# Kernel tuning notes

Hardware: AMD Instinct MI355X
Metric: run time of the kernel (lower is better)

## Reference

```python
import jax, jax.numpy as jnp
import numpy as np

EMBED_DIM = 512
NUM_HEADS = 8
HEAD_DIM = EMBED_DIM // NUM_HEADS
SCALING = HEAD_DIM ** (-0.5)
LAMBDA = 1.0
T = 128
B = 8


def setup_inputs() -> dict:
    key = jax.random.key(0)
    ks = jax.random.split(key, 8)
    d = EMBED_DIM
    # xavier-uniform-ish scale for weights
    w_lim = float(np.sqrt(6.0 / (3 * d + d)))
    o_lim = float(np.sqrt(6.0 / (d + d)))
    return {
        "query": jax.random.normal(ks[0], (T, B, d), jnp.float32),
        "key": jax.random.normal(ks[1], (T, B, d), jnp.float32),
        "value": jax.random.normal(ks[2], (T, B, d), jnp.float32),
        "correlation_bias": jax.random.normal(ks[3], (B, T, T, T), jnp.float32) * 0.1,
        "in_proj_weight": jax.random.uniform(ks[4], (3 * d, d), jnp.float32, -w_lim, w_lim),
        "in_proj_bias": jnp.zeros((3 * d,), jnp.float32),
        "out_w": jax.random.uniform(ks[5], (d, d), jnp.float32, -o_lim, o_lim),
        "out_b": jnp.zeros((d,), jnp.float32),
    }


def reference(query, key, value, correlation_bias, in_proj_weight, in_proj_bias, out_w, out_b):
    tgt_len, bsz, d = query.shape
    h, hd = NUM_HEADS, HEAD_DIM
    # split packed in-projection
    q = query @ in_proj_weight[:d].T + in_proj_bias[:d]
    k = key @ in_proj_weight[d:2 * d].T + in_proj_bias[d:2 * d]
    v = value @ in_proj_weight[2 * d:].T + in_proj_bias[2 * d:]
    q = q * SCALING
    # [T, B, D] -> [B*H, T, hd]
    q = q.reshape(tgt_len, bsz * h, hd).transpose(1, 0, 2)
    k = k.reshape(tgt_len, bsz * h, hd).transpose(1, 0, 2)
    v = v.reshape(tgt_len, bsz * h, hd).transpose(1, 0, 2)
    # trilinear score cube: [B*H, Tq, Tk, Tv]
    scores = jnp.einsum('iat,ibt,ict->iabc', q, k, v)
    # expand correlation bias over heads: [B,Tq,Tk,Tv] -> [B*H,Tq,Tk,Tv]
    bias = jnp.broadcast_to(
        correlation_bias[:, None], (bsz, h, tgt_len, tgt_len, tgt_len)
    ).reshape(bsz * h, tgt_len, tgt_len, tgt_len)
    scores = scores + LAMBDA * bias
    # mean/max fusion over Tv, softmax over Tk
    fused = jnp.mean(scores, axis=-1) + jnp.max(scores, axis=-1)
    w = jax.nn.softmax(fused.astype(jnp.float32), axis=-1).astype(fused.dtype)
    # bmm with q (note: attends over q itself, Tk == Tq required)
    attn = jnp.einsum('iab,ibd->iad', w, q)
    attn = attn.transpose(1, 0, 2).reshape(tgt_len, bsz, d)
    return attn @ out_w.T + out_b
```

## Files before the change

kernel.cpp:

```cpp
#include <hip/hip_runtime.h>
#include <math.h>

#define SCALING 0.125f

typedef __attribute__((ext_vector_type(8))) short short8;
typedef __attribute__((ext_vector_type(4))) float f32x4;

static __device__ __forceinline__ unsigned short bf16r(float x) {
  unsigned int u = __float_as_uint(x);
  u += 0x7fffu + ((u >> 16) & 1u);
  return (unsigned short)(u >> 16);
}
static __device__ __forceinline__ float bf16f(unsigned short h) {
  return __uint_as_float(((unsigned int)h) << 16);
}
static __device__ __forceinline__ unsigned int pk_bf16(float lo, float hi) {
  unsigned int ua = __float_as_uint(lo);
  unsigned int ub = __float_as_uint(hi);
  ua += 0x7fffu + ((ua >> 16) & 1u);
  ub += 0x7fffu + ((ub >> 16) & 1u);
  return __builtin_amdgcn_perm(ub, ua, 0x07060302u);
}
static __device__ __forceinline__ void split4(float4 x, ushort4& h, ushort4& l) {
  h.x = bf16r(x.x); l.x = bf16r(x.x - bf16f(h.x));
  h.y = bf16r(x.y); l.y = bf16r(x.y - bf16f(h.y));
  h.z = bf16r(x.z); l.z = bf16r(x.z - bf16f(h.z));
  h.w = bf16r(x.w); l.w = bf16r(x.w - bf16f(h.w));
}
union U4S8 { uint4 u; short8 s; };

__global__ __launch_bounds__(256)
void projmm_kernel(const float* __restrict__ query,
                   const float* __restrict__ key,
                   const float* __restrict__ value,
                   const float* __restrict__ W,
                   const float* __restrict__ bias,
                   float* __restrict__ qh, float* __restrict__ kh,
                   unsigned short* __restrict__ vh) {
  __shared__ __align__(16) unsigned short Ah[64 * 72];
  __shared__ __align__(16) unsigned short Al[64 * 72];
  __shared__ __align__(16) unsigned short Bh[64 * 72];
  __shared__ __align__(16) unsigned short Bl[64 * 72];
  const int n0 = blockIdx.x * 64;
  const int g = n0 >> 9;
  const float* __restrict__ X = (g == 0) ? query : (g == 1) ? key : value;
  const int m0 = blockIdx.y * 64;
  const int tid = threadIdx.x;
  const int w = tid >> 6, lane = tid & 63;
  const int quad = lane >> 4, n15 = lane & 15;
  const int srow = tid >> 2;
  const int scol = (tid & 3) * 16;

  f32x4 acc[4];
#pragma unroll
  for (int nt = 0; nt < 4; ++nt) acc[nt] = (f32x4){0.f, 0.f, 0.f, 0.f};

  float4 av[4], bv[4];
#pragma unroll
  for (int jj = 0; jj < 4; ++jj) {
    av[jj] = *(const float4*)&X[(m0 + srow) * 512 + scol + 4 * jj];
    bv[jj] = *(const float4*)&W[(n0 + srow) * 512 + scol + 4 * jj];
  }

  for (int k0 = 0; k0 < 512; k0 += 64) {
    __syncthreads();
#pragma unroll
    for (int jj = 0; jj < 4; ++jj) {
      ushort4 hh, ll;
      split4(av[jj], hh, ll);
      *(ushort4*)&Ah[srow * 72 + scol + 4 * jj] = hh;
      *(ushort4*)&Al[srow * 72 + scol + 4 * jj] = ll;
      split4(bv[jj], hh, ll);
      *(ushort4*)&Bh[srow * 72 + scol + 4 * jj] = hh;
      *(ushort4*)&Bl[srow * 72 + scol + 4 * jj] = ll;
    }
    __syncthreads();
    if (k0 + 64 < 512) {
#pragma unroll
      for (int jj = 0; jj < 4; ++jj) {
        av[jj] = *(const float4*)&X[(m0 + srow) * 512 + k0 + 64 + scol + 4 * jj];
        bv[jj] = *(const float4*)&W[(n0 + srow) * 512 + k0 + 64 + scol + 4 * jj];
      }
    }
#pragma unroll
    for (int kk = 0; kk < 2; ++kk) {
      short8 ah = *(const short8*)&Ah[(w * 16 + n15) * 72 + kk * 32 + quad * 8];
      short8 al = *(const short8*)&Al[(w * 16 + n15) * 72 + kk * 32 + quad * 8];
#pragma unroll
      for (int nt = 0; nt < 4; ++nt) {
        short8 bh = *(const short8*)&Bh[(nt * 16 + n15) * 72 + kk * 32 + quad * 8];
        short8 bl = *(const short8*)&Bl[(nt * 16 + n15) * 72 + kk * 32 + quad * 8];
        acc[nt] = __builtin_amdgcn_mfma_f32_16x16x32_bf16(ah, bh, acc[nt], 0, 0, 0);
        acc[nt] = __builtin_amdgcn_mfma_f32_16x16x32_bf16(ah, bl, acc[nt], 0, 0, 0);
        acc[nt] = __builtin_amdgcn_mfma_f32_16x16x32_bf16(al, bh, acc[nt], 0, 0, 0);
      }
    }
  }

#pragma unroll
  for (int nt = 0; nt < 4; ++nt) {
    const int j = n0 + nt * 16 + n15;
    const int jj = j & 511;
    const int head = jj >> 6;
    const int hd = jj & 63;
    const float bj = bias[j];
#pragma unroll
    for (int r = 0; r < 4; ++r) {
      const int row = m0 + w * 16 + quad * 4 + r;
      const int t = row >> 3;
      const int batch = row & 7;
      const int i = batch * 8 + head;
      const int idx = ((i << 7) + t) * 64 + hd;
      const float val = acc[nt][r] + bj;
      if (g == 0)      qh[idx] = val * SCALING;
      else if (g == 1) kh[idx] = val;
      else             vh[idx] = bf16r(val);
    }
  }
}

__global__ __launch_bounds__(256, 2)
void score_kernel(const float* __restrict__ qh,
                  const float* __restrict__ kh,
                  const unsigned short* __restrict__ vh,
                  const float* __restrict__ cbias,
                  float* __restrict__ attn) {
  __shared__ __align__(16) unsigned short Ks[2][128 * 72];
  __shared__ __align__(16) unsigned short Vs[2][128 * 72];
  __shared__ float rowS[8 * 128];

  const int ab = blockIdx.x;
  const int batch = ab >> 7;
  const int a = ab & 127;
  const int tid = threadIdx.x;
  const int w = tid >> 6;
  const int lane = tid & 63;
  const int quad = lane >> 4;
  const int n15 = lane & 15;
  const int col8 = (tid & 7) * 8;

  const float* __restrict__ bp = cbias + (size_t)ab * 16384;
  f32x4 biasReg[8][2];
#pragma unroll
  for (int ic = 0; ic < 8; ++ic)
#pragma unroll
    for (int jb = 0; jb < 2; ++jb) {
      const int b = w * 32 + jb * 16 + n15;
      biasReg[ic][jb] = *(const f32x4*)&bp[b * 128 + ic * 16 + quad * 4];
    }

  {
    const int i = batch * 8;
    const float* __restrict__ kb = kh + (size_t)i * 8192;
    const uint4* __restrict__ vb4 = (const uint4*)(vh + (size_t)i * 8192);
    const float* __restrict__ qa = qh + ((size_t)i * 128 + a) * 64;
    f32x4 q0 = *(const f32x4*)&qa[col8];
    f32x4 q1 = *(const f32x4*)&qa[col8 + 4];
#pragma unroll
    for (int j = 0; j < 4; ++j) {
      const int gg = j * 256 + tid;
      const int row = gg >> 3;
      *(uint4*)&Vs[0][row * 72 + col8] = vb4[gg];
      f32x4 k0 = *(const f32x4*)&kb[8 * gg];
      f32x4 k1 = *(const f32x4*)&kb[8 * gg + 4];
      k0 *= q0;
      k1 *= q1;
      uint4 pk;
      pk.x = pk_bf16(k0[0], k0[1]); pk.y = pk_bf16(k0[2], k0[3]);
      pk.z = pk_bf16(k1[0], k1[1]); pk.w = pk_bf16(k1[2], k1[3]);
      *(uint4*)&Ks[0][row * 72 + col8] = pk;
    }
  }
  __syncthreads();

  for (int h = 0; h < 8; ++h) {
    const int buf = h & 1;
    const int i = batch * 8 + h;

    uint4 vreg[4];
    f32x4 kreg[4][2];
    f32x4 qn0, qn1;
    if (h < 7) {
      const int in = i + 1;
      const float* __restrict__ kb = kh + (size_t)in * 8192;
      const uint4* __restrict__ vb4 = (const uint4*)(vh + (size_t)in * 8192);
      const float* __restrict__ qa = qh + ((size_t)in * 128 + a) * 64;
      qn0 = *(const f32x4*)&qa[col8];
      qn1 = *(const f32x4*)&qa[col8 + 4];
#pragma unroll
      for (int j = 0; j < 4; ++j) {
        const int gg = j * 256 + tid;
        vreg[j] = vb4[gg];
        kreg[j][0] = *(const f32x4*)&kb[8 * gg];
        kreg[j][1] = *(const f32x4*)&kb[8 * gg + 4];
      }
    }

    short8 bf[2][2];
#pragma unroll
    for (int jb = 0; jb < 2; ++jb)
#pragma unroll
      for (int kk = 0; kk < 2; ++kk)
        bf[jb][kk] = *(const short8*)&Ks[buf][(w * 32 + jb * 16 + n15) * 72 +
                                             kk * 32 + quad * 8];

    f32x4 acc[8][2];
#pragma unroll
    for (int ic = 0; ic < 8; ++ic)
#pragma unroll
      for (int jb = 0; jb < 2; ++jb) acc[ic][jb] = (f32x4){0.f, 0.f, 0.f, 0.f};
#pragma unroll
    for (int ic = 0; ic < 8; ++ic) {
      short8 a0 = *(const short8*)&Vs[buf][(ic * 16 + n15) * 72 + quad * 8];
      short8 a1 = *(const short8*)&Vs[buf][(ic * 16 + n15) * 72 + 32 + quad * 8];
      acc[ic][0] = __builtin_amdgcn_mfma_f32_16x16x32_bf16(a0, bf[0][0], acc[ic][0], 0, 0, 0);
      acc[ic][0] = __builtin_amdgcn_mfma_f32_16x16x32_bf16(a1, bf[0][1], acc[ic][0], 0, 0, 0);
      acc[ic][1] = __builtin_amdgcn_mfma_f32_16x16x32_bf16(a0, bf[1][0], acc[ic][1], 0, 0, 0);
      acc[ic][1] = __builtin_amdgcn_mfma_f32_16x16x32_bf16(a1, bf[1][1], acc[ic][1], 0, 0, 0);
    }

    if (h < 7) {
      const int nb = buf ^ 1;
#pragma unroll
      for (int j = 0; j < 4; ++j) {
        const int gg = j * 256 + tid;
        const int row = gg >> 3;
        *(uint4*)&Vs[nb][row * 72 + col8] = vreg[j];
        kreg[j][0] *= qn0;
        kreg[j][1] *= qn1;
        uint4 pk;
        pk.x = pk_bf16(kreg[j][0][0], kreg[j][0][1]);
        pk.y = pk_bf16(kreg[j][0][2], kreg[j][0][3]);
        pk.z = pk_bf16(kreg[j][1][0], kreg[j][1][1]);
        pk.w = pk_bf16(kreg[j][1][2], kreg[j][1][3]);
        *(uint4*)&Ks[nb][row * 72 + col8] = pk;
      }
    }

    float fsum[2] = {0.f, 0.f};
    float fmx[2] = {-INFINITY, -INFINITY};
#pragma unroll
    for (int ic = 0; ic < 8; ++ic)
#pragma unroll
      for (int jb = 0; jb < 2; ++jb) {
        const float v0 = acc[ic][jb][0] + biasReg[ic][jb][0];
        const float v1 = acc[ic][jb][1] + biasReg[ic][jb][1];
        const float v2 = acc[ic][jb][2] + biasReg[ic][jb][2];
        const float v3 = acc[ic][jb][3] + biasReg[ic][jb][3];
        fsum[jb] += (v0 + v1) + (v2 + v3);
        fmx[jb] = fmaxf(fmx[jb], fmaxf(fmaxf(v0, v1), fmaxf(v2, v3)));
      }
#pragma unroll
    for (int off = 16; off <= 32; off <<= 1) {
#pragma unroll
      for (int jb = 0; jb < 2; ++jb) {
        fsum[jb] += __shfl_xor(fsum[jb], off, 64);
        fmx[jb] = fmaxf(fmx[jb], __shfl_xor(fmx[jb], off, 64));
      }
    }
    if (quad == 0) {
      rowS[h * 128 + w * 32 + n15] = fsum[0] * (1.0f / 128.0f) + fmx[0];
      rowS[h * 128 + w * 32 + 16 + n15] = fsum[1] * (1.0f / 128.0f) + fmx[1];
    }

    __syncthreads();
  }

#pragma unroll
  for (int hh = 0; hh < 2; ++hh) {
    const int h = w * 2 + hh;
    const int i = batch * 8 + h;
    float f0 = rowS[h * 128 + lane], f1 = rowS[h * 128 + 64 + lane];
    float m = fmaxf(f0, f1);
#pragma unroll
    for (int off = 32; off >= 1; off >>= 1) m = fmaxf(m, __shfl_xor(m, off, 64));
    const float e0 = expf(f0 - m), e1 = expf(f1 - m);
    float s = e0 + e1;
#pragma unroll
    for (int off = 32; off >= 1; off >>= 1) s += __shfl_xor(s, off, 64);
    const float inv = 1.0f / s;
    rowS[h * 128 + lane] = e0 * inv;
    rowS[h * 128 + 64 + lane] = e1 * inv;
    const float* __restrict__ qp = qh + (size_t)i * 8192 + lane;
    float acc2 = 0.0f;
#pragma unroll 8
    for (int b = 0; b < 128; ++b)
      acc2 = fmaf(rowS[h * 128 + b], qp[b * 64], acc2);
    attn[((size_t)a * 8 + batch) * 512 + h * 64 + lane] = acc2;
  }
}

__global__ __launch_bounds__(256)
void outmm_kernel(const float* __restrict__ Xa,
                  const float* __restrict__ W,
                  const float* __restrict__ bias,
                  float* __restrict__ out) {
  __shared__ __align__(16) unsigned short Ah[64 * 72];
  __shared__ __align__(16) unsigned short Al[64 * 72];
  __shared__ __align__(16) unsigned short Bh[32 * 72];
  __shared__ __align__(16) unsigned short Bl[32 * 72];
  const int n0 = blockIdx.x * 32;
  const int m0 = blockIdx.y * 64;
  const int tid = threadIdx.x;
  const int w = tid >> 6, lane = tid & 63;
  const int quad = lane >> 4, n15 = lane & 15;
  const int srow = tid >> 2;
  const int scol = (tid & 3) * 16;
  const bool doB = tid >= 128;
  const int brow = (tid & 127) >> 2;
  const int bcol = (tid & 3) * 16;

  f32x4 acc[2];
#pragma unroll
  for (int nt = 0; nt < 2; ++nt) acc[nt] = (f32x4){0.f, 0.f, 0.f, 0.f};

  float4 av[4], bv[4];
#pragma unroll
  for (int jj = 0; jj < 4; ++jj)
    av[jj] = *(const float4*)&Xa[(m0 + srow) * 512 + scol + 4 * jj];
  if (doB) {
#pragma unroll
    for (int jj = 0; jj < 4; ++jj)
      bv[jj] = *(const float4*)&W[(n0 + brow) * 512 + bcol + 4 * jj];
  }

  for (int k0 = 0; k0 < 512; k0 += 64) {
    __syncthreads();
#pragma unroll
    for (int jj = 0; jj < 4; ++jj) {
      ushort4 hh, ll;
      split4(av[jj], hh, ll);
      *(ushort4*)&Ah[srow * 72 + scol + 4 * jj] = hh;
      *(ushort4*)&Al[srow * 72 + scol + 4 * jj] = ll;
    }
    if (doB) {
#pragma unroll
      for (int jj = 0; jj < 4; ++jj) {
        ushort4 hh, ll;
        split4(bv[jj], hh, ll);
        *(ushort4*)&Bh[brow * 72 + bcol + 4 * jj] = hh;
        *(ushort4*)&Bl[brow * 72 + bcol + 4 * jj] = ll;
      }
    }
    __syncthreads();
    if (k0 + 64 < 512) {
#pragma unroll
      for (int jj = 0; jj < 4; ++jj)
        av[jj] = *(const float4*)&Xa[(m0 + srow) * 512 + k0 + 64 + scol + 4 * jj];
      if (doB) {
#pragma unroll
        for (int jj = 0; jj < 4; ++jj)
          bv[jj] = *(const float4*)&W[(n0 + brow) * 512 + k0 + 64 + bcol + 4 * jj];
      }
    }
#pragma unroll
    for (int kk = 0; kk < 2; ++kk) {
      short8 ah = *(const short8*)&Ah[(w * 16 + n15) * 72 + kk * 32 + quad * 8];
      short8 al = *(const short8*)&Al[(w * 16 + n15) * 72 + kk * 32 + quad * 8];
#pragma unroll
      for (int nt = 0; nt < 2; ++nt) {
        short8 bh = *(const short8*)&Bh[(nt * 16 + n15) * 72 + kk * 32 + quad * 8];
        short8 bl = *(const short8*)&Bl[(nt * 16 + n15) * 72 + kk * 32 + quad * 8];
        acc[nt] = __builtin_amdgcn_mfma_f32_16x16x32_bf16(ah, bh, acc[nt], 0, 0, 0);
        acc[nt] = __builtin_amdgcn_mfma_f32_16x16x32_bf16(ah, bl, acc[nt], 0, 0, 0);
        acc[nt] = __builtin_amdgcn_mfma_f32_16x16x32_bf16(al, bh, acc[nt], 0, 0, 0);
      }
    }
  }

#pragma unroll
  for (int nt = 0; nt < 2; ++nt) {
    const int j = n0 + nt * 16 + n15;
    const float bj = bias[j];
#pragma unroll
    for (int r = 0; r < 4; ++r) {
      const int row = m0 + w * 16 + quad * 4 + r;
      out[(size_t)row * 512 + j] = acc[nt][r] + bj;
    }
  }
}

extern "C" void kernel_launch(void* const* d_in, const int* in_sizes, int n_in,
                              void* d_out, int out_size, void* d_ws,
                              size_t ws_size, hipStream_t stream) {
  const float* query = (const float*)d_in[0];
  const float* key   = (const float*)d_in[1];
  const float* value = (const float*)d_in[2];
  const float* cbias = (const float*)d_in[3];
  const float* W     = (const float*)d_in[4];
  const float* pb    = (const float*)d_in[5];
  const float* out_w = (const float*)d_in[6];
  const float* out_b = (const float*)d_in[7];
  float* out = (float*)d_out;

  float* ws = (float*)d_ws;
  float* qh = ws;
  float* kh = ws + 524288;
  unsigned short* vh = (unsigned short*)(ws + 1048576);
  float* attn = ws + 1048576 + 262144;

  projmm_kernel<<<dim3(24, 16), 256, 0, stream>>>(query, key, value, W, pb,
                                                  qh, kh, vh);
  score_kernel<<<1024, 256, 0, stream>>>(qh, kh, vh, cbias, attn);
  outmm_kernel<<<dim3(16, 16), 256, 0, stream>>>(attn, out_w, out_b, out);
}
```

Baseline: 187.2 us.

## Double score-kernel waves, keep K·q fragments in registers, seed MFMA with bias

```diff
diff --git a/kernel.cpp b/kernel.cpp
--- a/kernel.cpp
+++ b/kernel.cpp
@@ -119,13 +119,12 @@
   }
 }
 
-__global__ __launch_bounds__(256, 2)
+__global__ __launch_bounds__(512, 4)
 void score_kernel(const float* __restrict__ qh,
                   const float* __restrict__ kh,
                   const unsigned short* __restrict__ vh,
                   const float* __restrict__ cbias,
                   float* __restrict__ attn) {
-  __shared__ __align__(16) unsigned short Ks[2][128 * 72];
   __shared__ __align__(16) unsigned short Vs[2][128 * 72];
   __shared__ float rowS[8 * 128];
 
@@ -138,137 +137,106 @@
   const int quad = lane >> 4;
   const int n15 = lane & 15;
   const int col8 = (tid & 7) * 8;
+  const int brow = w * 16 + n15;
 
   const float* __restrict__ bp = cbias + (size_t)ab * 16384;
-  f32x4 biasReg[8][2];
+  f32x4 biasReg[8];
 #pragma unroll
   for (int ic = 0; ic < 8; ++ic)
-#pragma unroll
-    for (int jb = 0; jb < 2; ++jb) {
-      const int b = w * 32 + jb * 16 + n15;
-      biasReg[ic][jb] = *(const f32x4*)&bp[b * 128 + ic * 16 + quad * 4];
-    }
-
+    biasReg[ic] = *(const f32x4*)&bp[brow * 128 + ic * 16 + quad * 4];
+
+  short8 bf0, bf1;
   {
     const int i = batch * 8;
     const float* __restrict__ kb = kh + (size_t)i * 8192;
+    const float* __restrict__ qa = qh + ((size_t)i * 128 + a) * 64;
+    f32x4 k0a = *(const f32x4*)&kb[brow * 64 + quad * 8];
+    f32x4 k0b = *(const f32x4*)&kb[brow * 64 + quad * 8 + 4];
+    f32x4 k1a = *(const f32x4*)&kb[brow * 64 + 32 + quad * 8];
+    f32x4 k1b = *(const f32x4*)&kb[brow * 64 + 32 + quad * 8 + 4];
+    f32x4 q0a = *(const f32x4*)&qa[quad * 8];
+    f32x4 q0b = *(const f32x4*)&qa[quad * 8 + 4];
+    f32x4 q1a = *(const f32x4*)&qa[32 + quad * 8];
+    f32x4 q1b = *(const f32x4*)&qa[32 + quad * 8 + 4];
+    k0a *= q0a; k0b *= q0b; k1a *= q1a; k1b *= q1b;
+    U4S8 u0, u1;
+    u0.u.x = pk_bf16(k0a[0], k0a[1]); u0.u.y = pk_bf16(k0a[2], k0a[3]);
+    u0.u.z = pk_bf16(k0b[0], k0b[1]); u0.u.w = pk_bf16(k0b[2], k0b[3]);
+    u1.u.x = pk_bf16(k1a[0], k1a[1]); u1.u.y = pk_bf16(k1a[2], k1a[3]);
+    u1.u.z = pk_bf16(k1b[0], k1b[1]); u1.u.w = pk_bf16(k1b[2], k1b[3]);
+    bf0 = u0.s; bf1 = u1.s;
     const uint4* __restrict__ vb4 = (const uint4*)(vh + (size_t)i * 8192);
-    const float* __restrict__ qa = qh + ((size_t)i * 128 + a) * 64;
-    f32x4 q0 = *(const f32x4*)&qa[col8];
-    f32x4 q1 = *(const f32x4*)&qa[col8 + 4];
-#pragma unroll
-    for (int j = 0; j < 4; ++j) {
-      const int gg = j * 256 + tid;
-      const int row = gg >> 3;
-      *(uint4*)&Vs[0][row * 72 + col8] = vb4[gg];
-      f32x4 k0 = *(const f32x4*)&kb[8 * gg];
-      f32x4 k1 = *(const f32x4*)&kb[8 * gg + 4];
-      k0 *= q0;
-      k1 *= q1;
-      uint4 pk;
-      pk.x = pk_bf16(k0[0], k0[1]); pk.y = pk_bf16(k0[2], k0[3]);
-      pk.z = pk_bf16(k1[0], k1[1]); pk.w = pk_bf16(k1[2], k1[3]);
-      *(uint4*)&Ks[0][row * 72 + col8] = pk;
-    }
+    *(uint4*)&Vs[0][(tid >> 3) * 72 + col8] = vb4[tid];
+    *(uint4*)&Vs[0][(64 + (tid >> 3)) * 72 + col8] = vb4[512 + tid];
   }
   __syncthreads();
 
   for (int h = 0; h < 8; ++h) {
     const int buf = h & 1;
-    const int i = batch * 8 + h;
-
-    uint4 vreg[4];
-    f32x4 kreg[4][2];
-    f32x4 qn0, qn1;
+
+    uint4 vreg0, vreg1;
+    f32x4 kr0a, kr0b, kr1a, kr1b, qr0a, qr0b, qr1a, qr1b;
     if (h < 7) {
-      const int in = i + 1;
+      const int in = batch * 8 + h + 1;
       const float* __restrict__ kb = kh + (size_t)in * 8192;
+      const float* __restrict__ qa = qh + ((size_t)in * 128 + a) * 64;
       const uint4* __restrict__ vb4 = (const uint4*)(vh + (size_t)in * 8192);
-      const float* __restrict__ qa = qh + ((size_t)in * 128 + a) * 64;
-      qn0 = *(const f32x4*)&qa[col8];
-      qn1 = *(const f32x4*)&qa[col8 + 4];
-#pragma unroll
-      for (int j = 0; j < 4; ++j) {
-        const int gg = j * 256 + tid;
-        vreg[j] = vb4[gg];
-        kreg[j][0] = *(const f32x4*)&kb[8 * gg];
-        kreg[j][1] = *(const f32x4*)&kb[8 * gg + 4];
-      }
-    }
-
-    short8 bf[2][2];
-#pragma unroll
-    for (int jb = 0; jb < 2; ++jb)
-#pragma unroll
-      for (int kk = 0; kk < 2; ++kk)
-        bf[jb][kk] = *(const short8*)&Ks[buf][(w * 32 + jb * 16 + n15) * 72 +
-                                             kk * 32 + quad * 8];
-
-    f32x4 acc[8][2];
-#pragma unroll
-    for (int ic = 0; ic < 8; ++ic)
-#pragma unroll
-      for (int jb = 0; jb < 2; ++jb) acc[ic][jb] = (f32x4){0.f, 0.f, 0.f, 0.f};
+      vreg0 = vb4[tid];
+      vreg1 = vb4[512 + tid];
+      kr0a = *(const f32x4*)&kb[brow * 64 + quad * 8];
+      kr0b = *(const f32x4*)&kb[brow * 64 + quad * 8 + 4];
+      kr1a = *(const f32x4*)&kb[brow * 64 + 32 + quad * 8];
+      kr1b = *(const f32x4*)&kb[brow * 64 + 32 + quad * 8 + 4];
+      qr0a = *(const f32x4*)&qa[quad * 8];
+      qr0b = *(const f32x4*)&qa[quad * 8 + 4];
+      qr1a = *(const f32x4*)&qa[32 + quad * 8];
+      qr1b = *(const f32x4*)&qa[32 + quad * 8 + 4];
+    }
+
+    f32x4 acc[8];
 #pragma unroll
     for (int ic = 0; ic < 8; ++ic) {
       short8 a0 = *(const short8*)&Vs[buf][(ic * 16 + n15) * 72 + quad * 8];
       short8 a1 = *(const short8*)&Vs[buf][(ic * 16 + n15) * 72 + 32 + quad * 8];
-      acc[ic][0] = __builtin_amdgcn_mfma_f32_16x16x32_bf16(a0, bf[0][0], acc[ic][0], 0, 0, 0);
-      acc[ic][0] = __builtin_amdgcn_mfma_f32_16x16x32_bf16(a1, bf[0][1], acc[ic][0], 0, 0, 0);
-      acc[ic][1] = __builtin_amdgcn_mfma_f32_16x16x32_bf16(a0, bf[1][0], acc[ic][1], 0, 0, 0);
-      acc[ic][1] = __builtin_amdgcn_mfma_f32_16x16x32_bf16(a1, bf[1][1], acc[ic][1], 0, 0, 0);
+      f32x4 t = __builtin_amdgcn_mfma_f32_16x16x32_bf16(a0, bf0, biasReg[ic], 0, 0, 0);
+      acc[ic] = __builtin_amdgcn_mfma_f32_16x16x32_bf16(a1, bf1, t, 0, 0, 0);
     }
 
     if (h < 7) {
       const int nb = buf ^ 1;
-#pragma unroll
-      for (int j = 0; j < 4; ++j) {
-        const int gg = j * 256 + tid;
-        const int row = gg >> 3;
-        *(uint4*)&Vs[nb][row * 72 + col8] = vreg[j];
-        kreg[j][0] *= qn0;
-        kreg[j][1] *= qn1;
-        uint4 pk;
-        pk.x = pk_bf16(kreg[j][0][0], kreg[j][0][1]);
-        pk.y = pk_bf16(kreg[j][0][2], kreg[j][0][3]);
-        pk.z = pk_bf16(kreg[j][1][0], kreg[j][1][1]);
-        pk.w = pk_bf16(kreg[j][1][2], kreg[j][1][3]);
-        *(uint4*)&Ks[nb][row * 72 + col8] = pk;
-      }
-    }
-
-    float fsum[2] = {0.f, 0.f};
-    float fmx[2] = {-INFINITY, -INFINITY};
-#pragma unroll
-    for (int ic = 0; ic < 8; ++ic)
-#pragma unroll
-      for (int jb = 0; jb < 2; ++jb) {
-        const float v0 = acc[ic][jb][0] + biasReg[ic][jb][0];
-        const float v1 = acc[ic][jb][1] + biasReg[ic][jb][1];
-        const float v2 = acc[ic][jb][2] + biasReg[ic][jb][2];
-        const float v3 = acc[ic][jb][3] + biasReg[ic][jb][3];
-        fsum[jb] += (v0 + v1) + (v2 + v3);
-        fmx[jb] = fmaxf(fmx[jb], fmaxf(fmaxf(v0, v1), fmaxf(v2, v3)));
-      }
-#pragma unroll
-    for (int off = 16; off <= 32; off <<= 1) {
-#pragma unroll
-      for (int jb = 0; jb < 2; ++jb) {
-        fsum[jb] += __shfl_xor(fsum[jb], off, 64);
-        fmx[jb] = fmaxf(fmx[jb], __shfl_xor(fmx[jb], off, 64));
-      }
-    }
-    if (quad == 0) {
-      rowS[h * 128 + w * 32 + n15] = fsum[0] * (1.0f / 128.0f) + fmx[0];
-      rowS[h * 128 + w * 32 + 16 + n15] = fsum[1] * (1.0f / 128.0f) + fmx[1];
-    }
-
-    __syncthreads();
-  }
-
-#pragma unroll
-  for (int hh = 0; hh < 2; ++hh) {
-    const int h = w * 2 + hh;
+      *(uint4*)&Vs[nb][(tid >> 3) * 72 + col8] = vreg0;
+      *(uint4*)&Vs[nb][(64 + (tid >> 3)) * 72 + col8] = vreg1;
+      kr0a *= qr0a; kr0b *= qr0b; kr1a *= qr1a; kr1b *= qr1b;
+      U4S8 u0, u1;
+      u0.u.x = pk_bf16(kr0a[0], kr0a[1]); u0.u.y = pk_bf16(kr0a[2], kr0a[3]);
+      u0.u.z = pk_bf16(kr0b[0], kr0b[1]); u0.u.w = pk_bf16(kr0b[2], kr0b[3]);
+      u1.u.x = pk_bf16(kr1a[0], kr1a[1]); u1.u.y = pk_bf16(kr1a[2], kr1a[3]);
+      u1.u.z = pk_bf16(kr1b[0], kr1b[1]); u1.u.w = pk_bf16(kr1b[2], kr1b[3]);
+      bf0 = u0.s; bf1 = u1.s;
+    }
+
+    float fsum = 0.f;
+    float fmx = -INFINITY;
+#pragma unroll
+    for (int ic = 0; ic < 8; ++ic) {
+      const float v0 = acc[ic][0];
+      const float v1 = acc[ic][1];
+      const float v2 = acc[ic][2];
+      const float v3 = acc[ic][3];
+      fsum += (v0 + v1) + (v2 + v3);
+      fmx = fmaxf(fmx, fmaxf(fmaxf(v0, v1), fmaxf(v2, v3)));
+    }
+    fsum += __shfl_xor(fsum, 16, 64);
+    fmx = fmaxf(fmx, __shfl_xor(fmx, 16, 64));
+    fsum += __shfl_xor(fsum, 32, 64);
+    fmx = fmaxf(fmx, __shfl_xor(fmx, 32, 64));
+    if (quad == 0) rowS[h * 128 + w * 16 + n15] = fsum * (1.0f / 128.0f) + fmx;
+
+    __syncthreads();
+  }
+
+  {
+    const int h = w;
     const int i = batch * 8 + h;
     float f0 = rowS[h * 128 + lane], f1 = rowS[h * 128 + 64 + lane];
     float m = fmaxf(f0, f1);
@@ -401,6 +369,6 @@
 
   projmm_kernel<<<dim3(24, 16), 256, 0, stream>>>(query, key, value, W, pb,
                                                   qh, kh, vh);
-  score_kernel<<<1024, 256, 0, stream>>>(qh, kh, vh, cbias, attn);
+  score_kernel<<<1024, 512, 0, stream>>>(qh, kh, vh, cbias, attn);
   outmm_kernel<<<dim3(16, 16), 256, 0, stream>>>(attn, out_w, out_b, out);
 }
```

After: 194.2 us. 1.04x slower.

## Pre-split fp32 inputs and weights into bf16 hi/lo once before GEMMs

Applied to the files above, without the earlier changes.

```diff
diff --git a/kernel.cpp b/kernel.cpp
--- a/kernel.cpp
+++ b/kernel.cpp
@@ -30,10 +30,44 @@
 union U4S8 { uint4 u; short8 s; };
 
 __global__ __launch_bounds__(256)
-void projmm_kernel(const float* __restrict__ query,
-                   const float* __restrict__ key,
-                   const float* __restrict__ value,
-                   const float* __restrict__ W,
+void prep_kernel(const float* __restrict__ query,
+                 const float* __restrict__ key,
+                 const float* __restrict__ value,
+                 const float* __restrict__ W,
+                 const float* __restrict__ out_w,
+                 unsigned short* __restrict__ Xh,
+                 unsigned short* __restrict__ Xl,
+                 unsigned short* __restrict__ Wh,
+                 unsigned short* __restrict__ Wl,
+                 unsigned short* __restrict__ Owh,
+                 unsigned short* __restrict__ Owl) {
+  const int t = blockIdx.x * 256 + threadIdx.x;
+  const int e = t * 4;
+  const float* __restrict__ src;
+  unsigned short *dh, *dl;
+  if (e < 1572864) {
+    const int g = e >> 19, j = e & 524287;
+    src = (g == 0 ? query : g == 1 ? key : value) + j;
+    dh = Xh + e; dl = Xl + e;
+  } else if (e < 2359296) {
+    const int j = e - 1572864;
+    src = W + j; dh = Wh + j; dl = Wl + j;
+  } else {
+    const int j = e - 2359296;
+    src = out_w + j; dh = Owh + j; dl = Owl + j;
+  }
+  const float4 v = *(const float4*)src;
+  ushort4 hh, ll;
+  split4(v, hh, ll);
+  *(ushort4*)dh = hh;
+  *(ushort4*)dl = ll;
+}
+
+__global__ __launch_bounds__(256)
+void projmm_kernel(const unsigned short* __restrict__ Xh,
+                   const unsigned short* __restrict__ Xl,
+                   const unsigned short* __restrict__ Wh,
+                   const unsigned short* __restrict__ Wl,
                    const float* __restrict__ bias,
                    float* __restrict__ qh, float* __restrict__ kh,
                    unsigned short* __restrict__ vh) {
@@ -43,7 +77,8 @@
   __shared__ __align__(16) unsigned short Bl[64 * 72];
   const int n0 = blockIdx.x * 64;
   const int g = n0 >> 9;
-  const float* __restrict__ X = (g == 0) ? query : (g == 1) ? key : value;
+  const unsigned short* __restrict__ Xgh = Xh + g * 524288;
+  const unsigned short* __restrict__ Xgl = Xl + g * 524288;
   const int m0 = blockIdx.y * 64;
   const int tid = threadIdx.x;
   const int w = tid >> 6, lane = tid & 63;
@@ -55,32 +90,30 @@
 #pragma unroll
   for (int nt = 0; nt < 4; ++nt) acc[nt] = (f32x4){0.f, 0.f, 0.f, 0.f};
 
-  float4 av[4], bv[4];
-#pragma unroll
-  for (int jj = 0; jj < 4; ++jj) {
-    av[jj] = *(const float4*)&X[(m0 + srow) * 512 + scol + 4 * jj];
-    bv[jj] = *(const float4*)&W[(n0 + srow) * 512 + scol + 4 * jj];
+  uint4 rah0, rah1, ral0, ral1, rbh0, rbh1, rbl0, rbl1;
+  {
+    const int ar = (m0 + srow) * 512 + scol;
+    const int br = (n0 + srow) * 512 + scol;
+    rah0 = *(const uint4*)&Xgh[ar];     rah1 = *(const uint4*)&Xgh[ar + 8];
+    ral0 = *(const uint4*)&Xgl[ar];     ral1 = *(const uint4*)&Xgl[ar + 8];
+    rbh0 = *(const uint4*)&Wh[br];      rbh1 = *(const uint4*)&Wh[br + 8];
+    rbl0 = *(const uint4*)&Wl[br];      rbl1 = *(const uint4*)&Wl[br + 8];
   }
 
   for (int k0 = 0; k0 < 512; k0 += 64) {
     __syncthreads();
-#pragma unroll
-    for (int jj = 0; jj < 4; ++jj) {
-      ushort4 hh, ll;
-      split4(av[jj], hh, ll);
-      *(ushort4*)&Ah[srow * 72 + scol + 4 * jj] = hh;
-      *(ushort4*)&Al[srow * 72 + scol + 4 * jj] = ll;
-      split4(bv[jj], hh, ll);
-      *(ushort4*)&Bh[srow * 72 + scol + 4 * jj] = hh;
-      *(ushort4*)&Bl[srow * 72 + scol + 4 * jj] = ll;
-    }
+    *(uint4*)&Ah[srow * 72 + scol] = rah0; *(uint4*)&Ah[srow * 72 + scol + 8] = rah1;
+    *(uint4*)&Al[srow * 72 + scol] = ral0; *(uint4*)&Al[srow * 72 + scol + 8] = ral1;
+    *(uint4*)&Bh[srow * 72 + scol] = rbh0; *(uint4*)&Bh[srow * 72 + scol + 8] = rbh1;
+    *(uint4*)&Bl[srow * 72 + scol] = rbl0; *(uint4*)&Bl[srow * 72 + scol + 8] = rbl1;
     __syncthreads();
     if (k0 + 64 < 512) {
-#pragma unroll
-      for (int jj = 0; jj < 4; ++jj) {
-        av[jj] = *(const float4*)&X[(m0 + srow) * 512 + k0 + 64 + scol + 4 * jj];
-        bv[jj] = *(const float4*)&W[(n0 + srow) * 512 + k0 + 64 + scol + 4 * jj];
-      }
+      const int ar = (m0 + srow) * 512 + k0 + 64 + scol;
+      const int br = (n0 + srow) * 512 + k0 + 64 + scol;
+      rah0 = *(const uint4*)&Xgh[ar];   rah1 = *(const uint4*)&Xgh[ar + 8];
+      ral0 = *(const uint4*)&Xgl[ar];   ral1 = *(const uint4*)&Xgl[ar + 8];
+      rbh0 = *(const uint4*)&Wh[br];    rbh1 = *(const uint4*)&Wh[br + 8];
+      rbl0 = *(const uint4*)&Wl[br];    rbl1 = *(const uint4*)&Wl[br + 8];
     }
 #pragma unroll
     for (int kk = 0; kk < 2; ++kk) {
@@ -124,7 +157,8 @@
                   const float* __restrict__ kh,
                   const unsigned short* __restrict__ vh,
                   const float* __restrict__ cbias,
-                  float* __restrict__ attn) {
+                  unsigned short* __restrict__ attn_h,
+                  unsigned short* __restrict__ attn_l) {
   __shared__ __align__(16) unsigned short Ks[2][128 * 72];
   __shared__ __align__(16) unsigned short Vs[2][128 * 72];
   __shared__ float rowS[8 * 128];
@@ -286,13 +320,18 @@
 #pragma unroll 8
     for (int b = 0; b < 128; ++b)
       acc2 = fmaf(rowS[h * 128 + b], qp[b * 64], acc2);
-    attn[((size_t)a * 8 + batch) * 512 + h * 64 + lane] = acc2;
+    const size_t idx = ((size_t)a * 8 + batch) * 512 + h * 64 + lane;
+    const unsigned short hi = bf16r(acc2);
+    attn_h[idx] = hi;
+    attn_l[idx] = bf16r(acc2 - bf16f(hi));
   }
 }
 
 __global__ __launch_bounds__(256)
-void outmm_kernel(const float* __restrict__ Xa,
-                  const float* __restrict__ W,
+void outmm_kernel(const unsigned short* __restrict__ Xah,
+                  const unsigned short* __restrict__ Xal,
+                  const unsigned short* __restrict__ Owh,
+                  const unsigned short* __restrict__ Owl,
                   const float* __restrict__ bias,
                   float* __restrict__ out) {
   __shared__ __align__(16) unsigned short Ah[64 * 72];
@@ -314,43 +353,35 @@
 #pragma unroll
   for (int nt = 0; nt < 2; ++nt) acc[nt] = (f32x4){0.f, 0.f, 0.f, 0.f};
 
-  float4 av[4], bv[4];
-#pragma unroll
-  for (int jj = 0; jj < 4; ++jj)
-    av[jj] = *(const float4*)&Xa[(m0 + srow) * 512 + scol + 4 * jj];
+  uint4 rah0, rah1, ral0, ral1, rbh0, rbh1, rbl0, rbl1;
+  {
+    const int ar = (m0 + srow) * 512 + scol;
+    rah0 = *(const uint4*)&Xah[ar];   rah1 = *(const uint4*)&Xah[ar + 8];
+    ral0 = *(const uint4*)&Xal[ar];   ral1 = *(const uint4*)&Xal[ar + 8];
+  }
   if (doB) {
-#pragma unroll
-    for (int jj = 0; jj < 4; ++jj)
-      bv[jj] = *(const float4*)&W[(n0 + brow) * 512 + bcol + 4 * jj];
+    const int br = (n0 + brow) * 512 + bcol;
+    rbh0 = *(const uint4*)&Owh[br];   rbh1 = *(const uint4*)&Owh[br + 8];
+    rbl0 = *(const uint4*)&Owl[br];   rbl1 = *(const uint4*)&Owl[br + 8];
   }
 
   for (int k0 = 0; k0 < 512; k0 += 64) {
     __syncthreads();
-#pragma unroll
-    for (int jj = 0; jj < 4; ++jj) {
-      ushort4 hh, ll;
-      split4(av[jj], hh, ll);
-      *(ushort4*)&Ah[srow * 72 + scol + 4 * jj] = hh;
-      *(ushort4*)&Al[srow * 72 + scol + 4 * jj] = ll;
-    }
+    *(uint4*)&Ah[srow * 72 + scol] = rah0; *(uint4*)&Ah[srow * 72 + scol + 8] = rah1;
+    *(uint4*)&Al[srow * 72 + scol] = ral0; *(uint4*)&Al[srow * 72 + scol + 8] = ral1;
     if (doB) {
-#pragma unroll
-      for (int jj = 0; jj < 4; ++jj) {
-        ushort4 hh, ll;
-        split4(bv[jj], hh, ll);
-        *(ushort4*)&Bh[brow * 72 + bcol + 4 * jj] = hh;
-        *(ushort4*)&Bl[brow * 72 + bcol + 4 * jj] = ll;
-      }
+      *(uint4*)&Bh[brow * 72 + bcol] = rbh0; *(uint4*)&Bh[brow * 72 + bcol + 8] = rbh1;
+      *(uint4*)&Bl[brow * 72 + bcol] = rbl0; *(uint4*)&Bl[brow * 72 + bcol + 8] = rbl1;
     }
     __syncthreads();
     if (k0 + 64 < 512) {
-#pragma unroll
-      for (int jj = 0; jj < 4; ++jj)
-        av[jj] = *(const float4*)&Xa[(m0 + srow) * 512 + k0 + 64 + scol + 4 * jj];
+      const int ar = (m0 + srow) * 512 + k0 + 64 + scol;
+      rah0 = *(const uint4*)&Xah[ar]; rah1 = *(const uint4*)&Xah[ar + 8];
+      ral0 = *(const uint4*)&Xal[ar]; ral1 = *(const uint4*)&Xal[ar + 8];
       if (doB) {
-#pragma unroll
-        for (int jj = 0; jj < 4; ++jj)
-          bv[jj] = *(const float4*)&W[(n0 + brow) * 512 + k0 + 64 + bcol + 4 * jj];
+        const int br = (n0 + brow) * 512 + k0 + 64 + bcol;
+        rbh0 = *(const uint4*)&Owh[br]; rbh1 = *(const uint4*)&Owh[br + 8];
+        rbl0 = *(const uint4*)&Owl[br]; rbl1 = *(const uint4*)&Owl[br + 8];
       }
     }
 #pragma unroll
@@ -396,11 +427,21 @@
   float* ws = (float*)d_ws;
   float* qh = ws;
   float* kh = ws + 524288;
-  unsigned short* vh = (unsigned short*)(ws + 1048576);
-  float* attn = ws + 1048576 + 262144;
-
-  projmm_kernel<<<dim3(24, 16), 256, 0, stream>>>(query, key, value, W, pb,
+  unsigned short* vh     = (unsigned short*)(ws + 1048576);
+  unsigned short* attn_h = (unsigned short*)(ws + 1310720);
+  unsigned short* attn_l = (unsigned short*)(ws + 1572864);
+  unsigned short* Xh     = (unsigned short*)(ws + 1835008);
+  unsigned short* Xl     = (unsigned short*)(ws + 2621440);
+  unsigned short* Wh     = (unsigned short*)(ws + 3407872);
+  unsigned short* Wl     = (unsigned short*)(ws + 3801088);
+  unsigned short* Owh    = (unsigned short*)(ws + 4194304);
+  unsigned short* Owl    = (unsigned short*)(ws + 4325376);
+
+  prep_kernel<<<2560, 256, 0, stream>>>(query, key, value, W, out_w,
+                                        Xh, Xl, Wh, Wl, Owh, Owl);
+  projmm_kernel<<<dim3(24, 16), 256, 0, stream>>>(Xh, Xl, Wh, Wl, pb,
                                                   qh, kh, vh);
-  score_kernel<<<1024, 256, 0, stream>>>(qh, kh, vh, cbias, attn);
-  outmm_kernel<<<dim3(16, 16), 256, 0, stream>>>(attn, out_w, out_b, out);
-}
+  score_kernel<<<1024, 256, 0, stream>>>(qh, kh, vh, cbias, attn_h, attn_l);
+  outmm_kernel<<<dim3(16, 16), 256, 0, stream>>>(attn_h, attn_l, Owh, Owl,
+                                                 out_b, out);
+}
```

Result: faster. 182.2 us (-2.7%).
